# Kernel optimization log

Hardware: AMD Instinct MI355X
Metric: run time of the kernel (lower is better)

The kernel has to match this reference:

```python
import jax, jax.numpy as jnp
import numpy as np

N, D, E = 50000, 128, 800000
BN_EPS = 1e-5


def _gcn(x, W, b, row, col, val):
    # dropout with p=0.0 is identity; h = x @ W; out = adj @ h + b (COO SpMM)
    h = x @ W                                    # [N, d]
    msg = val[:, None] * h[col]                  # [E, d] gather + scale
    agg = jax.ops.segment_sum(msg, row, num_segments=x.shape[0])  # scatter-add
    return agg + b


def _predictor(x, W1, b1, gamma, beta, a, W2, b2):
    h = x @ W1 + b1
    mu = jnp.mean(h, axis=0)
    var = jnp.mean((h - mu) ** 2, axis=0)        # biased var (torch BN train mode)
    hn = (h - mu) / jnp.sqrt(var + BN_EPS) * gamma + beta
    hp = jnp.where(hn >= 0, hn, a * hn)          # PReLU, single shared alpha
    return hp @ W2 + b2


def _byol_loss(p, t):
    pn = p / jnp.linalg.norm(p, axis=-1, keepdims=True)
    tn = t / jnp.linalg.norm(t, axis=-1, keepdims=True)
    return 2.0 - 2.0 * jnp.sum(pn * tn, axis=-1)


def setup_inputs() -> dict:
    key = jax.random.key(0)
    ks = jax.random.split(key, 16)
    xavier = float(np.sqrt(6.0 / (D + D)))
    x = jax.random.normal(ks[0], (N, D), dtype=jnp.float32)
    perb = 0.05 * jax.random.normal(ks[1], (N, D), dtype=jnp.float32)
    edge_row = jax.random.randint(ks[2], (E,), 0, N, dtype=jnp.int32)
    edge_col = jax.random.randint(ks[3], (E,), 0, N, dtype=jnp.int32)
    edge_val = jax.random.uniform(ks[4], (E,), dtype=jnp.float32)
    W = jax.random.uniform(ks[5], (D, D), minval=-xavier, maxval=xavier, dtype=jnp.float32)
    b = jnp.zeros((D,), dtype=jnp.float32)
    # target encoder is a deepcopy at init; give it its own values to test the math
    Wt = jax.random.uniform(ks[6], (D, D), minval=-xavier, maxval=xavier, dtype=jnp.float32)
    bt = jnp.zeros((D,), dtype=jnp.float32)
    lin = float(1.0 / np.sqrt(D))
    W1 = jax.random.uniform(ks[7], (D, D), minval=-lin, maxval=lin, dtype=jnp.float32)
    b1 = jax.random.uniform(ks[8], (D,), minval=-lin, maxval=lin, dtype=jnp.float32)
    bn_gamma = jnp.ones((D,), dtype=jnp.float32)
    bn_beta = jnp.zeros((D,), dtype=jnp.float32)
    prelu_a = jnp.asarray(0.25, dtype=jnp.float32)
    W2 = jax.random.uniform(ks[9], (D, D), minval=-lin, maxval=lin, dtype=jnp.float32)
    b2 = jax.random.uniform(ks[10], (D,), minval=-lin, maxval=lin, dtype=jnp.float32)
    return dict(x=x, perb=perb, edge_row=edge_row, edge_col=edge_col, edge_val=edge_val,
                W=W, b=b, Wt=Wt, bt=bt, W1=W1, b1=b1, bn_gamma=bn_gamma,
                bn_beta=bn_beta, prelu_a=prelu_a, W2=W2, b2=b2)


def reference(x, perb, edge_row, edge_col, edge_val, W, b, Wt, bt,
              W1, b1, bn_gamma, bn_beta, prelu_a, W2, b2):
    x1 = x
    x2 = x + perb
    enc_x2 = _gcn(x2, W, b, edge_row, edge_col, edge_val)
    embed = x2 + enc_x2
    online_x = _gcn(x1, W, b, edge_row, edge_col, edge_val)
    online_y = enc_x2
    target_y = jax.lax.stop_gradient(_gcn(x1, Wt, bt, edge_row, edge_col, edge_val))
    target_x = jax.lax.stop_gradient(_gcn(x2, Wt, bt, edge_row, edge_col, edge_val))
    px = _predictor(online_x, W1, b1, bn_gamma, bn_beta, prelu_a, W2, b2)
    py = _predictor(online_y, W1, b1, bn_gamma, bn_beta, prelu_a, W2, b2)
    loss = jnp.mean(_byol_loss(px, target_x) + _byol_loss(py, target_y))
    return embed, loss
```

## Files before the change

### kernel.cpp

```cpp
#include <hip/hip_runtime.h>
#include <hip/hip_fp16.h>
#include <stdint.h>

typedef unsigned short u16;
typedef unsigned int u32;
typedef __attribute__((ext_vector_type(8))) short bf16x8;
typedef __attribute__((ext_vector_type(4))) short bf16x4;
typedef __attribute__((ext_vector_type(4))) float f32x4;

#define DD 128
#define CAP 64
#define STRA 136
#define STRC1 264
#define STRCF 132

__device__ __forceinline__ float bflo(u32 u){ return __uint_as_float(u<<16); }
__device__ __forceinline__ float bfhi(u32 u){ return __uint_as_float(u & 0xffff0000u); }
__device__ __forceinline__ float bf2f(u16 u){ return __uint_as_float(((u32)u)<<16); }
__device__ __forceinline__ u16 f2bf(float f){
  u32 u = __float_as_uint(f);
  return (u16)((u + 0x7fffu + ((u>>16)&1u)) >> 16);
}

#define FMA8(g, vv) do { \
    acc[0] += (vv)*bflo((g).x); acc[1] += (vv)*bfhi((g).x); \
    acc[2] += (vv)*bflo((g).y); acc[3] += (vv)*bfhi((g).y); \
    acc[4] += (vv)*bflo((g).z); acc[5] += (vv)*bfhi((g).z); \
    acc[6] += (vv)*bflo((g).w); acc[7] += (vv)*bfhi((g).w); } while(0)

__global__ __launch_bounds__(256) void kU_init(
    const float* __restrict__ x, const float* __restrict__ perb,
    const float* __restrict__ W, const float* __restrict__ Wt,
    const float* __restrict__ W1, const float* __restrict__ W2,
    u16* __restrict__ T, u16* __restrict__ Bswz,
    u16* __restrict__ W1swz, u16* __restrict__ W2swz,
    int* __restrict__ deg, float* __restrict__ stats,
    float* __restrict__ gbuf, int N)
{
  int f = blockIdx.x*256 + threadIdx.x;
  if (f < N) deg[f] = 0;
  if (f < 512) stats[f] = 0.f;
  if (f < 64) gbuf[f] = 0.f;
  if (f < 65536) {
    int idx = f;
    if (idx < 32768) {
      int j = idx & 7, lane = (idx>>3)&63, nt = (idx>>9)&15, kt = idx>>13;
      int k = kt*32 + (lane>>4)*8 + j, n = nt*16 + (lane&15);
      float v = (n < DD) ? W[k*DD + n] : Wt[k*DD + (n-DD)];
      Bswz[idx] = f2bf(v);
    } else {
      int t = idx - 32768;
      int which = t >> 14; t &= 16383;
      int j = t & 7, lane = (t>>3)&63, nt = (t>>9)&7, kt = (t>>12)&3;
      int k = kt*32 + (lane>>4)*8 + j, n = nt*16 + (lane&15);
      const float* __restrict__ src = which ? W2 : W1;
      u16* __restrict__ dst = which ? W2swz : W1swz;
      dst[t] = f2bf(src[k*DD + n]);
    }
  }
  if (f < N*32) {
    int r = f >> 5, c8 = f & 31;
    const float* src = (c8 < 16) ? (x + (size_t)r*DD + c8*8)
                                 : (perb + (size_t)r*DD + (c8-16)*8);
    float4 a = *(const float4*)src;
    float4 bq = *(const float4*)(src + 4);
    bf16x8 o;
    o[0]=(short)f2bf(a.x); o[1]=(short)f2bf(a.y); o[2]=(short)f2bf(a.z); o[3]=(short)f2bf(a.w);
    o[4]=(short)f2bf(bq.x); o[5]=(short)f2bf(bq.y); o[6]=(short)f2bf(bq.z); o[7]=(short)f2bf(bq.w);
    *(bf16x8*)(T + (size_t)r*256 + c8*8) = o;
  }
}

__global__ __launch_bounds__(256) void k2_bucket(
    const int* __restrict__ row, const int* __restrict__ col,
    const float* __restrict__ val, int E, int* __restrict__ deg,
    u32* __restrict__ perm, int* __restrict__ ovfc, int* __restrict__ ovf)
{
  int e = blockIdx.x*256 + threadIdx.x;
  if (e >= E) return;
  int r = row[e];
  int slot = atomicAdd(&deg[r], 1);
  if (slot < CAP) {
    u32 pk = (u32)(col[e] & 0xffff)
           | ((u32)__half_as_ushort(__float2half(val[e])) << 16);
    perm[(size_t)r*CAP + slot] = pk;
  }
  else { int oi = atomicAdd(ovfc, 1); if (oi < 4096) ovf[oi] = e; }
}

__global__ __launch_bounds__(256) void k3_spmm(
    const u32* __restrict__ perm, const int* __restrict__ deg,
    const u16* __restrict__ T, u16* __restrict__ T2, int N)
{
  int row = blockIdx.x*4 + (threadIdx.x >> 6);
  int l = threadIdx.x & 63;
  if (row >= N) return;
  int dg = deg[row];
  dg = dg < 0 ? 0 : (dg > CAP ? CAP : dg);
  const int half = l >> 5, hl = l & 31;
  const int eoff = hl * 8;
  float acc[8] = {0.f,0.f,0.f,0.f,0.f,0.f,0.f,0.f};
  for (int base = 0; base < dg; base += 64) {
    u32 pk = 0;
    if (base + l < dg) pk = perm[(size_t)row*CAP + base + l];
    int mm = dg - base; if (mm > 64) mm = 64;
    int kmax = (mm + 1) & ~1;
    int j = 0;
    for (; j + 8 <= kmax; j += 8) {
      u32 p0 = (u32)__shfl((int)pk, j + half);
      u32 p1 = (u32)__shfl((int)pk, j + 2 + half);
      u32 p2 = (u32)__shfl((int)pk, j + 4 + half);
      u32 p3 = (u32)__shfl((int)pk, j + 6 + half);
      int c0 = p0 & 0xffff; c0 = (c0 < N) ? c0 : 0;
      int c1 = p1 & 0xffff; c1 = (c1 < N) ? c1 : 0;
      int c2 = p2 & 0xffff; c2 = (c2 < N) ? c2 : 0;
      int c3 = p3 & 0xffff; c3 = (c3 < N) ? c3 : 0;
      float v0 = __half2float(__ushort_as_half((u16)(p0 >> 16)));
      float v1 = __half2float(__ushort_as_half((u16)(p1 >> 16)));
      float v2 = __half2float(__ushort_as_half((u16)(p2 >> 16)));
      float v3 = __half2float(__ushort_as_half((u16)(p3 >> 16)));
      uint4 g0 = *(const uint4*)(T + (size_t)c0*256 + eoff);
      uint4 g1 = *(const uint4*)(T + (size_t)c1*256 + eoff);
      uint4 g2 = *(const uint4*)(T + (size_t)c2*256 + eoff);
      uint4 g3 = *(const uint4*)(T + (size_t)c3*256 + eoff);
      FMA8(g0, v0); FMA8(g1, v1); FMA8(g2, v2); FMA8(g3, v3);
    }
    for (; j < kmax; j += 2) {
      u32 p0 = (u32)__shfl((int)pk, j + half);
      int c0 = p0 & 0xffff; c0 = (c0 < N) ? c0 : 0;
      float v0 = __half2float(__ushort_as_half((u16)(p0 >> 16)));
      uint4 g0 = *(const uint4*)(T + (size_t)c0*256 + eoff);
      FMA8(g0, v0);
    }
  }
  #pragma unroll
  for (int i = 0; i < 8; ++i) acc[i] += __shfl_xor(acc[i], 32);
  int sel = (hl >= 16) ? (hl - 16) : hl;
  bf16x8 ob;
  #pragma unroll
  for (int i = 0; i < 8; ++i) {
    float xv = __shfl(acc[i], sel);
    float o = (hl < 16) ? acc[i] : (xv + acc[i]);
    ob[i] = (short)f2bf(o);
  }
  if (half == 0)
    *(bf16x8*)(T2 + (size_t)row*256 + hl*8) = ob;
}

__global__ __launch_bounds__(256) void k3b_ovf(
    const int* __restrict__ rowI, const int* __restrict__ colI,
    const float* __restrict__ val, const int* __restrict__ ovfc,
    const int* __restrict__ ovf, const u16* __restrict__ T,
    u16* __restrict__ T2)
{
  int n = *ovfc; if (n > 4096) n = 4096;
  for (int i = 0; i < n; ++i) {
    int e = ovf[i];
    int r = rowI[e], c = colI[e];
    float v = val[e];
    int d = threadIdx.x;
    int dl = d & 127;
    float add = v * bf2f(T[(size_t)c*256 + dl]);
    if (d >= 128) add += v * bf2f(T[(size_t)c*256 + 128 + dl]);
    u16* p = &T2[(size_t)r*256 + d];
    *p = f2bf(bf2f(*p) + add);
  }
}

__global__ __launch_bounds__(256) void k4_gemm(
    const u16* __restrict__ T2, const u16* __restrict__ Bswz,
    const u16* __restrict__ W1swz,
    const float* __restrict__ b, const float* __restrict__ bt,
    const float* __restrict__ b1, const u16* __restrict__ T,
    u16* __restrict__ AGGb, float* __restrict__ outE,
    u16* __restrict__ Px, u16* __restrict__ Py,
    float* __restrict__ partial, int N, int NB)
{
  __shared__ __align__(16) u16 As1[64*STRA];
  __shared__ __align__(16) float CsU[64*STRCF];
  u16* Cs1 = (u16*)CsU;
  const int tid = threadIdx.x;
  const int r0 = blockIdx.x * 32;
  #pragma unroll
  for (int i = 0; i < 4; ++i) {
    int f = tid + 256*i;
    int row = f >> 4, c8 = f & 15;
    int r = r0 + (row & 31);
    bf16x8 ch = {0,0,0,0,0,0,0,0};
    if (r < N) ch = *(const bf16x8*)(T2 + (size_t)r*256 + (row>>5)*128 + c8*8);
    *(bf16x8*)&As1[row*STRA + c8*8] = ch;
  }
  __syncthreads();
  const int w = tid >> 6, l = tid & 63;
  const int m = l & 15, q = l >> 4;
  {
    f32x4 acc[16];
    #pragma unroll
    for (int nt = 0; nt < 16; ++nt) acc[nt] = (f32x4){0.f,0.f,0.f,0.f};
    const int arow = w*16 + m;
    #pragma unroll
    for (int kt = 0; kt < 4; ++kt) {
      bf16x8 af = *(const bf16x8*)&As1[arow*STRA + kt*32 + q*8];
      #pragma unroll
      for (int nt = 0; nt < 16; ++nt) {
        bf16x8 bfr = *(const bf16x8*)(Bswz + ((size_t)(kt*16+nt)*64 + l)*8);
        acc[nt] = __builtin_amdgcn_mfma_f32_16x16x32_bf16(af, bfr, acc[nt], 0, 0, 0);
      }
    }
    #pragma unroll
    for (int nt = 0; nt < 16; ++nt) {
      int n = nt*16 + m;
      float bv = (n < 128) ? b[n] : bt[n-128];
      #pragma unroll
      for (int i = 0; i < 4; ++i)
        Cs1[(w*16 + q*4 + i)*STRC1 + nt*16 + m] = f2bf(acc[nt][i] + bv);
    }
  }
  __syncthreads();
  {
    const int ar = tid >> 2, p = tid & 3;
    const int src = r0 + (ar & 31);
    if (src < N) {
      u16* dp = AGGb + (size_t)src*256 + (ar>>5)*128 + p*32;
      const u16* sp = &Cs1[ar*STRC1 + 128 + p*32];
      #pragma unroll
      for (int i = 0; i < 4; ++i)
        *(bf16x8*)(dp + i*8) = *(const bf16x8*)(sp + i*8);
    }
  }
  #pragma unroll
  for (int i = 0; i < 2; ++i) {
    int f = tid + 256*i;
    int rr = f >> 4, c8 = f & 15;
    int src = r0 + rr;
    if (src < N) {
      const u16* cp = &Cs1[(32+rr)*STRC1 + c8*8];
      bf16x8 xv = *(const bf16x8*)(T + (size_t)src*256 + c8*8);
      bf16x8 pv = *(const bf16x8*)(T + (size_t)src*256 + 128 + c8*8);
      bf16x8 cv = *(const bf16x8*)cp;
      float4 e0, e1;
      e0.x = bf2f((u16)xv[0])+bf2f((u16)pv[0])+bf2f((u16)cv[0]);
      e0.y = bf2f((u16)xv[1])+bf2f((u16)pv[1])+bf2f((u16)cv[1]);
      e0.z = bf2f((u16)xv[2])+bf2f((u16)pv[2])+bf2f((u16)cv[2]);
      e0.w = bf2f((u16)xv[3])+bf2f((u16)pv[3])+bf2f((u16)cv[3]);
      e1.x = bf2f((u16)xv[4])+bf2f((u16)pv[4])+bf2f((u16)cv[4]);
      e1.y = bf2f((u16)xv[5])+bf2f((u16)pv[5])+bf2f((u16)cv[5]);
      e1.z = bf2f((u16)xv[6])+bf2f((u16)pv[6])+bf2f((u16)cv[6]);
      e1.w = bf2f((u16)xv[7])+bf2f((u16)pv[7])+bf2f((u16)cv[7]);
      float* er = outE + (size_t)src*DD + c8*8;
      *(float4*)er = e0;
      *(float4*)(er+4) = e1;
    }
  }
  f32x4 acc2[8];
  #pragma unroll
  for (int nt = 0; nt < 8; ++nt) acc2[nt] = (f32x4){0.f,0.f,0.f,0.f};
  {
    const int arow = w*16 + m;
    #pragma unroll
    for (int kt = 0; kt < 4; ++kt) {
      bf16x8 af = *(const bf16x8*)&Cs1[arow*STRC1 + kt*32 + q*8];
      #pragma unroll
      for (int nt = 0; nt < 8; ++nt) {
        bf16x8 bfr = *(const bf16x8*)(W1swz + ((size_t)(kt*8+nt)*64 + l)*8);
        acc2[nt] = __builtin_amdgcn_mfma_f32_16x16x32_bf16(af, bfr, acc2[nt], 0, 0, 0);
      }
    }
  }
  __syncthreads();
  float* red = CsU;
  #pragma unroll
  for (int nt = 0; nt < 8; ++nt) {
    float bv = b1[nt*16 + m];
    float sum = 0.f, sq = 0.f;
    #pragma unroll
    for (int i = 0; i < 4; ++i) {
      int src = r0 + ((w*16 + q*4 + i) & 31);
      if (src < N) acc2[nt][i] += bv; else acc2[nt][i] = 0.f;
      sum += acc2[nt][i]; sq += acc2[nt][i]*acc2[nt][i];
    }
    sum += __shfl_xor(sum, 16); sum += __shfl_xor(sum, 32);
    sq  += __shfl_xor(sq, 16);  sq  += __shfl_xor(sq, 32);
    if (l < 16) {
      red[      w*128 + nt*16 + l] = sum;
      red[512 + w*128 + nt*16 + l] = sq;
    }
  }
  __syncthreads();
  {
    int type = tid >> 7, col = tid & 127;
    float v0 = red[type*512 +   0 + col] + red[type*512 + 128 + col];
    float v1 = red[type*512 + 256 + col] + red[type*512 + 384 + col];
    partial[((size_t)0*NB + blockIdx.x)*256 + tid] = v0;
    partial[((size_t)1*NB + blockIdx.x)*256 + tid] = v1;
  }
  __syncthreads();
  #pragma unroll
  for (int nt = 0; nt < 8; ++nt)
    #pragma unroll
    for (int i = 0; i < 4; ++i)
      CsU[(w*16 + q*4 + i)*STRCF + nt*16 + m] = acc2[nt][i];
  __syncthreads();
  {
    const int ar = tid >> 2, p = tid & 3;
    const int src = r0 + (ar & 31);
    if (src < N) {
      const float* sp = &CsU[ar*STRCF + p*32];
      u16* dp = ((ar >> 5) ? Py : Px) + (size_t)src*DD + p*32;
      #pragma unroll
      for (int i = 0; i < 4; ++i) {
        bf16x8 ob;
        #pragma unroll
        for (int t2 = 0; t2 < 8; ++t2) ob[t2] = (short)f2bf(sp[i*8+t2]);
        *(bf16x8*)(dp + i*8) = ob;
      }
    }
  }
}

__global__ __launch_bounds__(256) void k5b_stats(
    const float* __restrict__ partial, float* __restrict__ stats, int nb)
{
  int seg = blockIdx.y, chunk = blockIdx.x, t = threadIdx.x;
  int per = (nb + gridDim.x - 1) / gridDim.x;
  int lo = chunk*per, hi = lo+per; if (hi > nb) hi = nb;
  float s = 0.f;
  const float* p = partial + (size_t)seg*nb*256;
  for (int i = lo; i < hi; ++i) s += p[(size_t)i*256 + t];
  atomicAdd(&stats[seg*256 + t], s);
}

__global__ __launch_bounds__(256) void k6_gemm_loss(
    const u16* __restrict__ Px, const u16* __restrict__ Py,
    const u16* __restrict__ AGGb, const float* __restrict__ stats,
    const float* __restrict__ gamma, const float* __restrict__ beta,
    const float* __restrict__ aP, const u16* __restrict__ W2swz,
    const float* __restrict__ b2, float* __restrict__ gloss, int N)
{
  __shared__ __align__(16) float Cs[64*STRCF];
  u16* As = (u16*)Cs;
  __shared__ float s1s[128], s2s[128];
  __shared__ float gred[4];
  const int tid = threadIdx.x;
  const int seg = blockIdx.y;
  const u16* __restrict__ P = seg ? Py : Px;
  const int toff = seg ? 0 : 128;
  const float invN = 1.f / (float)N;
  if (tid < 128) {
    float mu = stats[seg*256 + tid] * invN;
    float var = stats[seg*256 + 128 + tid] * invN - mu*mu;
    float rstd = rsqrtf(var + 1e-5f);
    float s1 = rstd * gamma[tid];
    s1s[tid] = s1;
    s2s[tid] = beta[tid] - mu*s1;
  }
  const float alpha = aP[0];
  const int r0 = blockIdx.x * 64;
  __syncthreads();
  #pragma unroll
  for (int i = 0; i < 4; ++i) {
    int f = tid + 256*i;
    int row = f >> 4, c8 = f & 15;
    int r = r0 + row;
    bf16x8 ch = {0,0,0,0,0,0,0,0};
    if (r < N) ch = *(const bf16x8*)(P + (size_t)r*DD + c8*8);
    bf16x8 a;
    #pragma unroll
    for (int t2 = 0; t2 < 8; ++t2) {
      int colc = c8*8 + t2;
      float hv = bf2f((u16)ch[t2]);
      float hn = hv*s1s[colc] + s2s[colc];
      hn = hn >= 0.f ? hn : alpha*hn;
      a[t2] = (short)f2bf(hn);
    }
    *(bf16x8*)&As[row*STRA + c8*8] = a;
  }
  __syncthreads();
  const int w = tid >> 6, l = tid & 63;
  const int m = l & 15, q = l >> 4;
  f32x4 acc[8];
  #pragma unroll
  for (int nt = 0; nt < 8; ++nt) acc[nt] = (f32x4){0.f,0.f,0.f,0.f};
  const int arow = w*16 + m;
  #pragma unroll
  for (int kt = 0; kt < 4; ++kt) {
    bf16x8 af = *(const bf16x8*)&As[arow*STRA + kt*32 + q*8];
    #pragma unroll
    for (int nt = 0; nt < 8; ++nt) {
      bf16x8 bfr = *(const bf16x8*)(W2swz + ((size_t)(kt*8+nt)*64 + l)*8);
      acc[nt] = __builtin_amdgcn_mfma_f32_16x16x32_bf16(af, bfr, acc[nt], 0, 0, 0);
    }
  }
  __syncthreads();
  #pragma unroll
  for (int nt = 0; nt < 8; ++nt) {
    float bv = b2[nt*16 + m];
    #pragma unroll
    for (int i = 0; i < 4; ++i)
      Cs[(w*16 + q*4 + i)*STRCF + nt*16 + m] = acc[nt][i] + bv;
  }
  __syncthreads();
  {
    const int rt = tid >> 2, qq = tid & 3;
    const int r = r0 + rt;
    float pp = 0.f, tt = 0.f, pt = 0.f;
    if (r < N) {
      const float* prow = &Cs[rt*STRCF + qq*32];
      const u16* trow = AGGb + (size_t)r*256 + toff + qq*32;
      #pragma unroll
      for (int i = 0; i < 4; ++i) {
        float4 pa = *(const float4*)(prow + i*8);
        float4 pb = *(const float4*)(prow + i*8 + 4);
        uint4 twv = *(const uint4*)(trow + i*8);
        float t0=bflo(twv.x), t1=bfhi(twv.x), t2=bflo(twv.y), t3=bfhi(twv.y);
        float t4=bflo(twv.z), t5=bfhi(twv.z), t6=bflo(twv.w), t7=bfhi(twv.w);
        pp += pa.x*pa.x + pa.y*pa.y + pa.z*pa.z + pa.w*pa.w
            + pb.x*pb.x + pb.y*pb.y + pb.z*pb.z + pb.w*pb.w;
        tt += t0*t0 + t1*t1 + t2*t2 + t3*t3 + t4*t4 + t5*t5 + t6*t6 + t7*t7;
        pt += pa.x*t0 + pa.y*t1 + pa.z*t2 + pa.w*t3
            + pb.x*t4 + pb.y*t5 + pb.z*t6 + pb.w*t7;
      }
    }
    pp += __shfl_xor(pp, 1); pp += __shfl_xor(pp, 2);
    tt += __shfl_xor(tt, 1); tt += __shfl_xor(tt, 2);
    pt += __shfl_xor(pt, 1); pt += __shfl_xor(pt, 2);
    float lsum = (r < N) ? (2.f - 2.f * pt * rsqrtf(pp * tt)) : 0.f;
    lsum += __shfl_xor(lsum, 4);  lsum += __shfl_xor(lsum, 8);
    lsum += __shfl_xor(lsum, 16); lsum += __shfl_xor(lsum, 32);
    if (l == 0) gred[w] = lsum;
  }
  __syncthreads();
  if (tid == 0) atomicAdd(gloss, gred[0]+gred[1]+gred[2]+gred[3]);
}

__global__ void k7_loss(const float* __restrict__ gloss, float* __restrict__ out, int N, int total)
{
  out[total] = gloss[0] / (float)N;
}

extern "C" void kernel_launch(void* const* d_in, const int* in_sizes, int n_in,
                              void* d_out, int out_size, void* d_ws, size_t ws_size,
                              hipStream_t stream)
{
  const float* x    = (const float*)d_in[0];
  const float* perb = (const float*)d_in[1];
  const int*   erow = (const int*)d_in[2];
  const int*   ecol = (const int*)d_in[3];
  const float* eval_= (const float*)d_in[4];
  const float* W    = (const float*)d_in[5];
  const float* b    = (const float*)d_in[6];
  const float* Wt   = (const float*)d_in[7];
  const float* bt   = (const float*)d_in[8];
  const float* W1   = (const float*)d_in[9];
  const float* b1   = (const float*)d_in[10];
  const float* gam  = (const float*)d_in[11];
  const float* bet  = (const float*)d_in[12];
  const float* aP   = (const float*)d_in[13];
  const float* W2   = (const float*)d_in[14];
  const float* b2   = (const float*)d_in[15];
  const int N = in_sizes[0] / DD;
  const int E = in_sizes[2];
  const int NB4 = (N + 31)/32;
  const int NB5 = (N + 63)/64;

  char* ws = (char*)d_ws;
  size_t off = 0;
  auto alloc = [&](size_t bytes) -> void* {
    void* p = ws + off;
    off += (bytes + 255) & ~(size_t)255;
    return p;
  };
  u16*   AGGb = (u16*)  alloc((size_t)N*256*sizeof(u16));
  u16*   T    = (u16*)  alloc((size_t)N*256*sizeof(u16));
  u16*   T2   = (u16*)  alloc((size_t)N*256*sizeof(u16));
  u16*   Px   = (u16*)  alloc((size_t)N*DD*sizeof(u16));
  u16*   Py   = (u16*)  alloc((size_t)N*DD*sizeof(u16));
  int*   deg  = (int*)  alloc((size_t)N*sizeof(int));
  float* stats= (float*)alloc(512*sizeof(float));
  float* gloss= (float*)alloc(256);
  int*   ovfc = (int*)((char*)gloss + 64);
  u32*   perm = (u32*)  alloc((size_t)N*CAP*sizeof(u32));
  int*   ovf  = (int*)  alloc(4096*sizeof(int));
  u16*   Bswz = (u16*)  alloc(32768*sizeof(u16));
  u16*   W1swz= (u16*)  alloc(16384*sizeof(u16));
  u16*   W2swz= (u16*)  alloc(16384*sizeof(u16));
  float* partial = (float*)alloc((size_t)2*NB4*256*sizeof(float));
  if (ws_size < off) return;

  kU_init<<<(N*32 + 255)/256, 256, 0, stream>>>(x, perb, W, Wt, W1, W2,
                                                T, Bswz, W1swz, W2swz,
                                                deg, stats, gloss, N);
  k2_bucket<<<(E + 255)/256, 256, 0, stream>>>(erow, ecol, eval_, E, deg, perm, ovfc, ovf);
  k3_spmm<<<(N + 3)/4, 256, 0, stream>>>(perm, deg, T, T2, N);
  k3b_ovf<<<1, 256, 0, stream>>>(erow, ecol, eval_, ovfc, ovf, T, T2);
  k4_gemm<<<NB4, 256, 0, stream>>>(T2, Bswz, W1swz, b, bt, b1, T,
                                   AGGb, (float*)d_out, Px, Py, partial, N, NB4);
  k5b_stats<<<dim3(16, 2), 256, 0, stream>>>(partial, stats, NB4);
  k6_gemm_loss<<<dim3(NB5, 2), 256, 0, stream>>>(Px, Py, AGGb, stats, gam, bet, aP,
                                                 W2swz, b2, gloss, N);
  k7_loss<<<1, 1, 0, stream>>>(gloss, (float*)d_out, N, N*DD);
}
```

Measured before the change: 332.1 us.

## Split k4 GEMM into two 128-column passes to cut registers and LDS

The first GEMM in k4_gemm used to compute all 256 output columns at once, with 16 accumulator tiles and a 64x264 shared staging buffer. It now runs two 8-tile passes, target half first and then online half, and reuses one 64x136 bf16 tile buffer. The reduction scratch is aliased onto the input tile, and launch bounds ask for 4 blocks per SM, all to lower VGPR and LDS use so more blocks fit on each CU. In exchange the A tile is read from LDS twice, extra barriers are added, and the output-staging sync is removed; that last change relies on the barrier after the reduction writes.

After: 332.5 us. Within noise of the previous version (+0.1%).

```diff
diff --git a/kernel.cpp b/kernel.cpp
--- a/kernel.cpp
+++ b/kernel.cpp
@@ -11,7 +11,6 @@
 #define DD 128
 #define CAP 64
 #define STRA 136
-#define STRC1 264
 #define STRCF 132
 
 __device__ __forceinline__ float bflo(u32 u){ return __uint_as_float(u<<16); }
@@ -167,7 +166,7 @@
   }
 }
 
-__global__ __launch_bounds__(256) void k4_gemm(
+__global__ __launch_bounds__(256, 4) void k4_gemm(
     const u16* __restrict__ T2, const u16* __restrict__ Bswz,
     const u16* __restrict__ W1swz,
     const float* __restrict__ b, const float* __restrict__ bt,
@@ -177,8 +176,7 @@
     float* __restrict__ partial, int N, int NB)
 {
   __shared__ __align__(16) u16 As1[64*STRA];
-  __shared__ __align__(16) float CsU[64*STRCF];
-  u16* Cs1 = (u16*)CsU;
+  __shared__ __align__(16) u16 Ct[64*STRA];
   const int tid = threadIdx.x;
   const int r0 = blockIdx.x * 32;
   #pragma unroll
@@ -193,28 +191,25 @@
   __syncthreads();
   const int w = tid >> 6, l = tid & 63;
   const int m = l & 15, q = l >> 4;
-  {
-    f32x4 acc[16];
-    #pragma unroll
-    for (int nt = 0; nt < 16; ++nt) acc[nt] = (f32x4){0.f,0.f,0.f,0.f};
-    const int arow = w*16 + m;
-    #pragma unroll
-    for (int kt = 0; kt < 4; ++kt) {
-      bf16x8 af = *(const bf16x8*)&As1[arow*STRA + kt*32 + q*8];
-      #pragma unroll
-      for (int nt = 0; nt < 16; ++nt) {
-        bf16x8 bfr = *(const bf16x8*)(Bswz + ((size_t)(kt*16+nt)*64 + l)*8);
-        acc[nt] = __builtin_amdgcn_mfma_f32_16x16x32_bf16(af, bfr, acc[nt], 0, 0, 0);
-      }
-    }
-    #pragma unroll
-    for (int nt = 0; nt < 16; ++nt) {
-      int n = nt*16 + m;
-      float bv = (n < 128) ? b[n] : bt[n-128];
-      #pragma unroll
-      for (int i = 0; i < 4; ++i)
-        Cs1[(w*16 + q*4 + i)*STRC1 + nt*16 + m] = f2bf(acc[nt][i] + bv);
-    }
+  const int arow = w*16 + m;
+  f32x4 acc[8];
+  #pragma unroll
+  for (int nt = 0; nt < 8; ++nt) acc[nt] = (f32x4){0.f,0.f,0.f,0.f};
+  #pragma unroll
+  for (int kt = 0; kt < 4; ++kt) {
+    bf16x8 af = *(const bf16x8*)&As1[arow*STRA + kt*32 + q*8];
+    #pragma unroll
+    for (int nt = 0; nt < 8; ++nt) {
+      bf16x8 bfr = *(const bf16x8*)(Bswz + ((size_t)(kt*16 + 8 + nt)*64 + l)*8);
+      acc[nt] = __builtin_amdgcn_mfma_f32_16x16x32_bf16(af, bfr, acc[nt], 0, 0, 0);
+    }
+  }
+  #pragma unroll
+  for (int nt = 0; nt < 8; ++nt) {
+    float bv = bt[nt*16 + m];
+    #pragma unroll
+    for (int i = 0; i < 4; ++i)
+      Ct[(w*16 + q*4 + i)*STRA + nt*16 + m] = f2bf(acc[nt][i] + bv);
   }
   __syncthreads();
   {
@@ -222,19 +217,39 @@
     const int src = r0 + (ar & 31);
     if (src < N) {
       u16* dp = AGGb + (size_t)src*256 + (ar>>5)*128 + p*32;
-      const u16* sp = &Cs1[ar*STRC1 + 128 + p*32];
+      const u16* sp = &Ct[ar*STRA + p*32];
       #pragma unroll
       for (int i = 0; i < 4; ++i)
         *(bf16x8*)(dp + i*8) = *(const bf16x8*)(sp + i*8);
     }
   }
+  __syncthreads();
+  #pragma unroll
+  for (int nt = 0; nt < 8; ++nt) acc[nt] = (f32x4){0.f,0.f,0.f,0.f};
+  #pragma unroll
+  for (int kt = 0; kt < 4; ++kt) {
+    bf16x8 af = *(const bf16x8*)&As1[arow*STRA + kt*32 + q*8];
+    #pragma unroll
+    for (int nt = 0; nt < 8; ++nt) {
+      bf16x8 bfr = *(const bf16x8*)(Bswz + ((size_t)(kt*16 + nt)*64 + l)*8);
+      acc[nt] = __builtin_amdgcn_mfma_f32_16x16x32_bf16(af, bfr, acc[nt], 0, 0, 0);
+    }
+  }
+  #pragma unroll
+  for (int nt = 0; nt < 8; ++nt) {
+    float bv = b[nt*16 + m];
+    #pragma unroll
+    for (int i = 0; i < 4; ++i)
+      Ct[(w*16 + q*4 + i)*STRA + nt*16 + m] = f2bf(acc[nt][i] + bv);
+  }
+  __syncthreads();
   #pragma unroll
   for (int i = 0; i < 2; ++i) {
     int f = tid + 256*i;
     int rr = f >> 4, c8 = f & 15;
     int src = r0 + rr;
     if (src < N) {
-      const u16* cp = &Cs1[(32+rr)*STRC1 + c8*8];
+      const u16* cp = &Ct[(32+rr)*STRA + c8*8];
       bf16x8 xv = *(const bf16x8*)(T + (size_t)src*256 + c8*8);
       bf16x8 pv = *(const bf16x8*)(T + (size_t)src*256 + 128 + c8*8);
       bf16x8 cv = *(const bf16x8*)cp;
@@ -252,23 +267,18 @@
       *(float4*)(er+4) = e1;
     }
   }
-  f32x4 acc2[8];
-  #pragma unroll
-  for (int nt = 0; nt < 8; ++nt) acc2[nt] = (f32x4){0.f,0.f,0.f,0.f};
-  {
-    const int arow = w*16 + m;
-    #pragma unroll
-    for (int kt = 0; kt < 4; ++kt) {
-      bf16x8 af = *(const bf16x8*)&Cs1[arow*STRC1 + kt*32 + q*8];
-      #pragma unroll
-      for (int nt = 0; nt < 8; ++nt) {
-        bf16x8 bfr = *(const bf16x8*)(W1swz + ((size_t)(kt*8+nt)*64 + l)*8);
-        acc2[nt] = __builtin_amdgcn_mfma_f32_16x16x32_bf16(af, bfr, acc2[nt], 0, 0, 0);
-      }
-    }
-  }
-  __syncthreads();
-  float* red = CsU;
+  #pragma unroll
+  for (int nt = 0; nt < 8; ++nt) acc[nt] = (f32x4){0.f,0.f,0.f,0.f};
+  #pragma unroll
+  for (int kt = 0; kt < 4; ++kt) {
+    bf16x8 af = *(const bf16x8*)&Ct[arow*STRA + kt*32 + q*8];
+    #pragma unroll
+    for (int nt = 0; nt < 8; ++nt) {
+      bf16x8 bfr = *(const bf16x8*)(W1swz + ((size_t)(kt*8+nt)*64 + l)*8);
+      acc[nt] = __builtin_amdgcn_mfma_f32_16x16x32_bf16(af, bfr, acc[nt], 0, 0, 0);
+    }
+  }
+  float* red = (float*)As1;
   #pragma unroll
   for (int nt = 0; nt < 8; ++nt) {
     float bv = b1[nt*16 + m];
@@ -276,8 +286,8 @@
     #pragma unroll
     for (int i = 0; i < 4; ++i) {
       int src = r0 + ((w*16 + q*4 + i) & 31);
-      if (src < N) acc2[nt][i] += bv; else acc2[nt][i] = 0.f;
-      sum += acc2[nt][i]; sq += acc2[nt][i]*acc2[nt][i];
+      if (src < N) acc[nt][i] += bv; else acc[nt][i] = 0.f;
+      sum += acc[nt][i]; sq += acc[nt][i]*acc[nt][i];
     }
     sum += __shfl_xor(sum, 16); sum += __shfl_xor(sum, 32);
     sq  += __shfl_xor(sq, 16);  sq  += __shfl_xor(sq, 32);
@@ -294,26 +304,21 @@
     partial[((size_t)0*NB + blockIdx.x)*256 + tid] = v0;
     partial[((size_t)1*NB + blockIdx.x)*256 + tid] = v1;
   }
-  __syncthreads();
   #pragma unroll
   for (int nt = 0; nt < 8; ++nt)
     #pragma unroll
     for (int i = 0; i < 4; ++i)
-      CsU[(w*16 + q*4 + i)*STRCF + nt*16 + m] = acc2[nt][i];
+      Ct[(w*16 + q*4 + i)*STRA + nt*16 + m] = f2bf(acc[nt][i]);
   __syncthreads();
   {
     const int ar = tid >> 2, p = tid & 3;
     const int src = r0 + (ar & 31);
     if (src < N) {
-      const float* sp = &CsU[ar*STRCF + p*32];
+      const u16* sp = &Ct[ar*STRA + p*32];
       u16* dp = ((ar >> 5) ? Py : Px) + (size_t)src*DD + p*32;
       #pragma unroll
-      for (int i = 0; i < 4; ++i) {
-        bf16x8 ob;
-        #pragma unroll
-        for (int t2 = 0; t2 < 8; ++t2) ob[t2] = (short)f2bf(sp[i*8+t2]);
-        *(bf16x8*)(dp + i*8) = ob;
-      }
+      for (int i = 0; i < 4; ++i)
+        *(bf16x8*)(dp + i*8) = *(const bf16x8*)(sp + i*8);
     }
   }
 }
```
